# Optimization experiments

Measured on AMD Instinct MI355X. Metric: run time of the kernel, lower is better.

Reference implementation:

```python
import jax, jax.numpy as jnp
import numpy as np

B, S, D, H, DH = 2, 2048, 1024, 16, 64

def setup_inputs() -> dict:
    key = jax.random.key(0)
    ks = jax.random.split(key, 9)
    sc = 0.02
    return {
        "x":  jax.random.normal(ks[0], (B, S, D), jnp.float32),
        "Wq": jax.random.normal(ks[1], (H, D, DH), jnp.float32) * sc,
        "bq": jax.random.normal(ks[2], (H, DH), jnp.float32) * sc,
        "Wk": jax.random.normal(ks[3], (H, D, DH), jnp.float32) * sc,
        "bk": jax.random.normal(ks[4], (H, DH), jnp.float32) * sc,
        "Wv": jax.random.normal(ks[5], (H, D, DH), jnp.float32) * sc,
        "bv": jax.random.normal(ks[6], (H, DH), jnp.float32) * sc,
        "Wo": jax.random.normal(ks[7], (D, D), jnp.float32) * sc,
        "bo": jax.random.normal(ks[8], (D,), jnp.float32) * sc,
    }

def reference(x, Wq, bq, Wk, bk, Wv, bv, Wo, bo):
    # Fused version of the per-head Python loop: all H heads batched.
    # q,k,v: [B,H,S,DH]
    q = jnp.einsum("bsi,hid->bhsd", x, Wq) + bq[None, :, None, :]
    k = jnp.einsum("bsi,hid->bhsd", x, Wk) + bk[None, :, None, :]
    v = jnp.einsum("bsi,hid->bhsd", x, Wv) + bv[None, :, None, :]
    scale = 1.0 / jnp.sqrt(jnp.asarray(DH, x.dtype))
    scores = jnp.einsum("bhsd,bhtd->bhst", q, k) * scale  # [B,H,S,S]
    attn = jax.nn.softmax(scores, axis=-1)
    o = jnp.einsum("bhst,bhtd->bhsd", attn, v)            # [B,H,S,DH]
    # torch.cat([head_0,...,head_{H-1}], dim=-1) -> [B,S,H*DH]
    o = jnp.transpose(o, (0, 2, 1, 3)).reshape(B, S, H * DH)
    # Dropout is identity in eval mode; final dense projection.
    return jnp.einsum("bsi,io->bso", o, Wo) + bo
```

## Files before the change

### kernel.cpp

```cpp
#include <hip/hip_runtime.h>
#include <hip/hip_bf16.h>

#define BB 2
#define SS 2048
#define DD 1024
#define HH 16
#define DHH 64

typedef __attribute__((ext_vector_type(8))) __bf16 bf16x8;
typedef __attribute__((ext_vector_type(4))) float f32x4;
typedef __attribute__((ext_vector_type(16))) float f32x16;
typedef __attribute__((ext_vector_type(4))) int i32x4;
typedef __attribute__((ext_vector_type(4))) unsigned int u32x4;

#define MFMA16 __builtin_amdgcn_mfma_f32_16x16x32_bf16
#define MFMA32 __builtin_amdgcn_mfma_f32_32x32x16_bf16

__device__ __forceinline__ unsigned short f2b(float f) {
  __hip_bfloat16 h = __float2bfloat16(f);
  unsigned short u;
  __builtin_memcpy(&u, &h, 2);
  return u;
}

__device__ __forceinline__ float b2f(unsigned short u) {
  unsigned int x = ((unsigned int)u) << 16;
  float f;
  __builtin_memcpy(&f, &x, 4);
  return f;
}

__device__ __forceinline__ float exp2_fast(float x) {
  float r;
  asm("v_exp_f32 %0, %1" : "=v"(r) : "v"(x));
  return r;
}

__device__ __forceinline__ unsigned int cvtpk_bf16(float lo_, float hi_) {
  unsigned int r;
  asm("v_cvt_pk_bf16_f32 %0, %1, %2" : "=v"(r) : "v"(lo_), "v"(hi_));
  return r;
}

__device__ __forceinline__ void gl_lds16(const void* g, void* l) {
  __builtin_amdgcn_global_load_lds((const __attribute__((address_space(1))) void*)g,
                                   (__attribute__((address_space(3))) void*)l, 16, 0, 0);
}

__global__ __launch_bounds__(256) void k_prep(const float* __restrict__ x,
                                              const float* __restrict__ Wq,
                                              const float* __restrict__ Wk,
                                              const float* __restrict__ Wv,
                                              const float* __restrict__ Wo,
                                              unsigned short* __restrict__ xb,
                                              unsigned short* __restrict__ wqkvt,
                                              unsigned short* __restrict__ wot) {
  int blk = blockIdx.x;
  if (blk < 4096) {
    int i = blk * 256 + threadIdx.x;
    float4 v = ((const float4*)x)[i];
    ushort4 o;
    o.x = f2b(v.x); o.y = f2b(v.y); o.z = f2b(v.z); o.w = f2b(v.w);
    ((ushort4*)xb)[i] = o;
    return;
  }
  __shared__ float t[32][33];
  const float* im;
  unsigned short* om;
  int R, C, c0, r0;
  if (blk < 7168) {
    int bi2 = blk - 4096;
    int z = bi2 >> 6, rem = bi2 & 63;
    im = (z < 16 ? Wq : (z < 32 ? Wk : Wv)) + (size_t)(z & 15) * DD * DHH;
    om = wqkvt + (size_t)z * DD * DHH;
    R = DD; C = DHH;
    c0 = (rem & 1) * 32; r0 = (rem >> 1) * 32;
  } else {
    int bi2 = blk - 7168;
    im = Wo; om = wot;
    R = DD; C = DD;
    c0 = (bi2 & 31) * 32; r0 = (bi2 >> 5) * 32;
  }
  int tx = threadIdx.x & 31, ty = threadIdx.x >> 5;
#pragma unroll
  for (int rr = ty; rr < 32; rr += 8)
    t[rr][tx] = im[(size_t)(r0 + rr) * C + c0 + tx];
  __syncthreads();
#pragma unroll
  for (int rr = ty; rr < 32; rr += 8)
    om[(size_t)(c0 + rr) * R + r0 + tx] = f2b(t[tx][rr]);
}

__global__ __launch_bounds__(256) void k_qkv(const unsigned short* __restrict__ A,
                                             const unsigned short* __restrict__ Wt,
                                             const float* __restrict__ bq,
                                             const float* __restrict__ bk,
                                             const float* __restrict__ bv,
                                             unsigned short* __restrict__ Qb,
                                             unsigned short* __restrict__ Kb,
                                             unsigned short* __restrict__ Vtb) {
  __shared__ __align__(16) unsigned short SMEM[128 * 64 + 64 * 64];
  unsigned short* As = SMEM;
  unsigned short* Bs = SMEM + 128 * 64;
  int tid = threadIdx.x;
  int w = tid >> 6, l = tid & 63, lr = l & 15, lg = l >> 4;
  int col0 = blockIdx.x * 64, row0 = blockIdx.y * 128;
  int sel = col0 >> 10;
  bool vsel = (sel == 2);
  const float* biasp = sel == 0 ? bq : (sel == 1 ? bk : bv);
  unsigned short* outp = sel == 0 ? Qb : Kb;
  float qscale = sel == 0 ? 0.18033688011112042f : 1.0f;

  int r8 = l >> 3, c8 = l & 7;
  const unsigned short* Ab = A + (size_t)(row0 + w * 32 + r8) * DD + c8 * 8;
  const unsigned short* Bb = Wt + (size_t)(col0 + w * 16 + r8) * DD + c8 * 8;

  f32x4 zero = {0.f, 0.f, 0.f, 0.f};
  f32x4 acc[2][4];
#pragma unroll
  for (int m = 0; m < 2; m++)
#pragma unroll
    for (int n = 0; n < 4; n++) acc[m][n] = zero;

  for (int k0 = 0; k0 < DD; k0 += 64) {
    __syncthreads();
#pragma unroll
    for (int c = 0; c < 4; c++)
      gl_lds16(Ab + (size_t)c * 8 * DD + k0, (char*)As + (w * 32 + c * 8) * 128);
#pragma unroll
    for (int c = 0; c < 2; c++)
      gl_lds16(Bb + (size_t)c * 8 * DD + k0, (char*)Bs + (w * 16 + c * 8) * 128);
    __syncthreads();
#pragma unroll
    for (int kk = 0; kk < 2; kk++) {
      bf16x8 af[2], bfr[4];
#pragma unroll
      for (int m = 0; m < 2; m++)
        af[m] = *(const bf16x8*)&As[(w * 32 + m * 16 + lr) * 64 + kk * 32 + lg * 8];
#pragma unroll
      for (int n = 0; n < 4; n++)
        bfr[n] = *(const bf16x8*)&Bs[(n * 16 + lr) * 64 + kk * 32 + lg * 8];
      if (!vsel) {
#pragma unroll
        for (int m = 0; m < 2; m++)
#pragma unroll
          for (int n = 0; n < 4; n++)
            acc[m][n] = MFMA16(af[m], bfr[n], acc[m][n], 0, 0, 0);
      } else {
#pragma unroll
        for (int m = 0; m < 2; m++)
#pragma unroll
          for (int n = 0; n < 4; n++)
            acc[m][n] = MFMA16(bfr[n], af[m], acc[m][n], 0, 0, 0);
      }
    }
  }

  __syncthreads();
  unsigned short* Ts = SMEM;
  if (!vsel) {
#pragma unroll
    for (int n = 0; n < 4; n++) {
      int cl = n * 16 + lr;
      float bias = biasp[(col0 + cl) & 1023];
#pragma unroll
      for (int m = 0; m < 2; m++) {
#pragma unroll
        for (int j = 0; j < 4; j++) {
          int sl = w * 32 + m * 16 + lg * 4 + j;
          Ts[sl * 72 + cl] = f2b((acc[m][n][j] + bias) * qscale);
        }
      }
    }
    __syncthreads();
    int trow = tid >> 3, tc = tid & 7;
#pragma unroll
    for (int pass = 0; pass < 4; pass++) {
      int sl = pass * 32 + trow;
      int c0l = tc * 8;
      i32x4 v = *(const i32x4*)&Ts[sl * 72 + c0l];
      int c = col0 + c0l;
      int hh = (c >> 6) & 15, d = c & 63;
      int row = row0 + sl;
      int b = row >> 11, s = row & 2047;
      *(i32x4*)(outp + ((size_t)(b * HH + hh) * SS + s) * DHH + d) = v;
    }
  } else {
#pragma unroll
    for (int n = 0; n < 4; n++) {
#pragma unroll
      for (int j = 0; j < 4; j++) {
        int cl = n * 16 + lg * 4 + j;
        float bias = bv[((col0 & 1023) + cl) & 1023];
#pragma unroll
        for (int m = 0; m < 2; m++) {
          int sl = w * 32 + m * 16 + lr;
          Ts[cl * 136 + sl] = f2b(acc[m][n][j] + bias);
        }
      }
    }
    __syncthreads();
    int trow = tid >> 4, tc = tid & 15;
    int b = row0 >> 11, s0 = row0 & 2047;
#pragma unroll
    for (int pass = 0; pass < 4; pass++) {
      int cl = pass * 16 + trow;
      int s8 = tc * 8;
      i32x4 v = *(const i32x4*)&Ts[cl * 136 + s8];
      int cg = (col0 & 1023) + cl;
      *(i32x4*)(Vtb + (size_t)(b * 1024 + cg) * SS + s0 + s8) = v;
    }
  }
}

__global__ __launch_bounds__(256) void k_proj(const unsigned short* __restrict__ A,
                                              const unsigned short* __restrict__ Wt,
                                              const float* __restrict__ bo,
                                              float* __restrict__ out) {
  __shared__ __align__(16) unsigned short As[64 * 64];
  __shared__ __align__(16) unsigned short Bs[64 * 64];
  int tid = threadIdx.x;
  int w = tid >> 6, l = tid & 63, lr = l & 15, lg = l >> 4;
  int col0 = blockIdx.x * 64, row0 = blockIdx.y * 64;

  int r8 = l >> 3, c8 = l & 7;
  const unsigned short* Ab = A + (size_t)(row0 + w * 16 + r8) * DD + c8 * 8;
  const unsigned short* Bb = Wt + (size_t)(col0 + w * 16 + r8) * DD + c8 * 8;

  f32x4 zero = {0.f, 0.f, 0.f, 0.f};
  f32x4 acc[4];
#pragma unroll
  for (int n = 0; n < 4; n++) acc[n] = zero;

  for (int k0 = 0; k0 < DD; k0 += 64) {
    __syncthreads();
#pragma unroll
    for (int c = 0; c < 2; c++) {
      gl_lds16(Ab + (size_t)c * 8 * DD + k0, (char*)As + (w * 16 + c * 8) * 128);
      gl_lds16(Bb + (size_t)c * 8 * DD + k0, (char*)Bs + (w * 16 + c * 8) * 128);
    }
    __syncthreads();
#pragma unroll
    for (int kk = 0; kk < 2; kk++) {
      bf16x8 af = *(const bf16x8*)&As[(w * 16 + lr) * 64 + kk * 32 + lg * 8];
      bf16x8 bfr[4];
#pragma unroll
      for (int n = 0; n < 4; n++)
        bfr[n] = *(const bf16x8*)&Bs[(n * 16 + lr) * 64 + kk * 32 + lg * 8];
#pragma unroll
      for (int n = 0; n < 4; n++)
        acc[n] = MFMA16(af, bfr[n], acc[n], 0, 0, 0);
    }
  }

#pragma unroll
  for (int n = 0; n < 4; n++) {
    int c = col0 + n * 16 + lr;
    float bias = bo[c];
#pragma unroll
    for (int j = 0; j < 4; j++) {
      int row = row0 + w * 16 + lg * 4 + j;
      out[(size_t)row * DD + c] = acc[n][j] + bias;
    }
  }
}

#define QT 128
#define KVB 64

__global__ __launch_bounds__(256, 4) void k_attn(const unsigned short* __restrict__ Q,
                                                 const unsigned short* __restrict__ K,
                                                 const unsigned short* __restrict__ Vt,
                                                 unsigned short* __restrict__ Opart,
                                                 float* __restrict__ lse) {
  __shared__ __align__(16) char sm[32768];

  int tid = threadIdx.x;
  int w = tid >> 6, lane = tid & 63;
  int q32 = lane & 31, hi = lane >> 5;
  int r8 = lane >> 3, c8 = lane & 7;
  int cg = c8 ^ r8;

  int n = blockIdx.x;
  int bh = ((n & 7) << 2) | ((n >> 3) & 3);
  int rest = n >> 5;
  int q0 = (rest & 15) * QT;
  int chunk = rest >> 4;
  int kvbase = chunk * (SS / 2);

  const unsigned short* Qm = Q + (size_t)bh * SS * DHH;
  const unsigned short* Km = K + (size_t)bh * SS * DHH;
  const unsigned short* Vm = Vt + (size_t)bh * DHH * SS;

  bf16x8 qf[4];
  {
    const unsigned short* qrow = Qm + (size_t)(q0 + w * 32 + q32) * DHH + hi * 8;
#pragma unroll
    for (int ks = 0; ks < 4; ks++)
      qf[ks] = *(const bf16x8*)(qrow + ks * 16);
  }

#pragma unroll
  for (int c = 0; c < 2; c++) {
    int rr = w * 16 + c * 8 + r8;
    gl_lds16(Km + (size_t)(kvbase + rr) * DHH + cg * 8, sm + (w * 16 + c * 8) * 128);
    gl_lds16(Vm + (size_t)rr * SS + kvbase + cg * 8, sm + 16384 + (w * 16 + c * 8) * 128);
  }
  __syncthreads();

  f32x16 oacc0 = {}, oacc1 = {};
  float m_ = -1e30f, l_ = 0.f;
  const int swq = (q32 & 7) << 4;

  for (int t = 0; t < SS / 2 / KVB; t++) {
    const char* Kc = sm + (t & 1) * 8192;
    const char* Vc = sm + 16384 + (t & 1) * 8192;

    if (t + 1 < SS / 2 / KVB) {
      int kv0 = kvbase + (t + 1) * KVB;
      char* kd = sm + ((t + 1) & 1) * 8192;
      char* vd = sm + 16384 + ((t + 1) & 1) * 8192;
#pragma unroll
      for (int c = 0; c < 2; c++) {
        int rr = w * 16 + c * 8 + r8;
        gl_lds16(Km + (size_t)(kv0 + rr) * DHH + cg * 8, kd + (w * 16 + c * 8) * 128);
        gl_lds16(Vm + (size_t)rr * SS + kv0 + cg * 8, vd + (w * 16 + c * 8) * 128);
      }
    }

    f32x16 p0 = {}, p1 = {};
    __builtin_amdgcn_s_setprio(1);
#pragma unroll
    for (int ks = 0; ks < 4; ks++) {
      int co = (ks * 32 + hi * 16) ^ swq;
      bf16x8 kf0 = *(const bf16x8*)(Kc + q32 * 128 + co);
      bf16x8 kf1 = *(const bf16x8*)(Kc + (32 + q32) * 128 + co);
      p0 = MFMA32(kf0, qf[ks], p0, 0, 0, 0);
      p1 = MFMA32(kf1, qf[ks], p1, 0, 0, 0);
    }
    __builtin_amdgcn_s_setprio(0);

    float t8[8];
#pragma unroll
    for (int r = 0; r < 8; r++)
      t8[r] = fmaxf(fmaxf(p0[r], p0[r + 8]), fmaxf(p1[r], p1[r + 8]));
#pragma unroll
    for (int r = 0; r < 4; r++) t8[r] = fmaxf(t8[r], t8[r + 4]);
    float tmax = fmaxf(fmaxf(t8[0], t8[1]), fmaxf(t8[2], t8[3]));
    tmax = fmaxf(tmax, __shfl_xor(tmax, 32));

    if (__any(tmax > m_ + 8.0f)) {
      float nm = fmaxf(m_, tmax);
      float al = exp2_fast(m_ - nm);
      m_ = nm; l_ *= al;
#pragma unroll
      for (int r = 0; r < 16; r++) { oacc0[r] *= al; oacc1[r] *= al; }
    }

#pragma unroll
    for (int r = 0; r < 16; r++) p0[r] = exp2_fast(p0[r] - m_);
#pragma unroll
    for (int r = 0; r < 16; r++) p1[r] = exp2_fast(p1[r] - m_);
    float s8[8];
#pragma unroll
    for (int r = 0; r < 8; r++) s8[r] = (p0[r] + p0[r + 8]) + (p1[r] + p1[r + 8]);
#pragma unroll
    for (int r = 0; r < 4; r++) s8[r] += s8[r + 4];
    l_ += ((s8[0] + s8[1]) + (s8[2] + s8[3]));

    __builtin_amdgcn_s_setprio(1);
    u32x4 pa;
#define MKPA(PB, u) do { \
    unsigned int a0 = cvtpk_bf16(PB[8*(u)+0], PB[8*(u)+1]); \
    unsigned int a1 = cvtpk_bf16(PB[8*(u)+2], PB[8*(u)+3]); \
    unsigned int b0 = cvtpk_bf16(PB[8*(u)+4], PB[8*(u)+5]); \
    unsigned int b1 = cvtpk_bf16(PB[8*(u)+6], PB[8*(u)+7]); \
    asm("v_permlane32_swap_b32 %0, %1" : "+v"(a0), "+v"(b0)); \
    asm("v_permlane32_swap_b32 %0, %1" : "+v"(a1), "+v"(b1)); \
    pa[0] = a0; pa[1] = a1; pa[2] = b0; pa[3] = b1; \
  } while (0)
#define PVSTEP(s) do { \
    bf16x8 pf = *(bf16x8*)&pa; \
    bf16x8 vf0 = *(const bf16x8*)(Vc + q32 * 128 + (((s) * 32 + hi * 16) ^ swq)); \
    bf16x8 vf1 = *(const bf16x8*)(Vc + (32 + q32) * 128 + (((s) * 32 + hi * 16) ^ swq)); \
    oacc0 = MFMA32(vf0, pf, oacc0, 0, 0, 0); \
    oacc1 = MFMA32(vf1, pf, oacc1, 0, 0, 0); \
  } while (0)
    MKPA(p0, 0); PVSTEP(0);
    MKPA(p0, 1); PVSTEP(1);
    MKPA(p1, 0); PVSTEP(2);
    MKPA(p1, 1); PVSTEP(3);
#undef MKPA
#undef PVSTEP
    __builtin_amdgcn_s_setprio(0);

    __syncthreads();
  }

  l_ += __shfl_xor(l_, 32);
  float invl = 1.0f / l_;
  float lsev = m_ + __log2f(l_);
  __syncthreads();
  unsigned short* Os = (unsigned short*)sm;
  int rowq = w * 32 + q32;
#pragma unroll
  for (int r = 0; r < 16; r++) {
    int d = (r & 3) + 8 * (r >> 2) + 4 * hi;
    Os[rowq * 72 + d] = f2b(oacc0[r] * invl);
    Os[rowq * 72 + 32 + d] = f2b(oacc1[r] * invl);
  }
  if (hi == 0) lse[((size_t)chunk * 32 + bh) * SS + q0 + rowq] = lsev;
  __syncthreads();
#pragma unroll
  for (int i = 0; i < 4; i++) {
    int ci = tid + i * 256;
    int r = ci >> 3, c = ci & 7;
    i32x4 v = *(const i32x4*)&Os[r * 72 + c * 8];
    *(i32x4*)(Opart + (((size_t)chunk * 32 + bh) * SS + q0 + r) * DHH + c * 8) = v;
  }
}

__global__ __launch_bounds__(256) void k_comb(const unsigned short* __restrict__ Opart,
                                              const float* __restrict__ lse,
                                              unsigned short* __restrict__ Ocat) {
  int g = blockIdx.x * 256 + threadIdx.x;
  int row = g >> 3;
  int d8 = (g & 7) * 8;
  int bh = row >> 11, q = row & 2047;
  int bi = bh >> 4, h = bh & 15;
  float e0 = lse[row], e1 = lse[BB * HH * SS + row];
  float mx = fmaxf(e0, e1);
  float w0 = exp2_fast(e0 - mx), w1 = exp2_fast(e1 - mx);
  float inv = 1.0f / (w0 + w1);
  w0 *= inv; w1 *= inv;
  const unsigned short* P0 = Opart + (size_t)row * DHH + d8;
  const unsigned short* P1 = P0 + (size_t)BB * HH * SS * DHH;
  ushort4 a0 = *(const ushort4*)P0, a1 = *(const ushort4*)(P0 + 4);
  ushort4 b0 = *(const ushort4*)P1, b1 = *(const ushort4*)(P1 + 4);
  ushort4 o0, o1;
  o0.x = f2b(w0 * b2f(a0.x) + w1 * b2f(b0.x));
  o0.y = f2b(w0 * b2f(a0.y) + w1 * b2f(b0.y));
  o0.z = f2b(w0 * b2f(a0.z) + w1 * b2f(b0.z));
  o0.w = f2b(w0 * b2f(a0.w) + w1 * b2f(b0.w));
  o1.x = f2b(w0 * b2f(a1.x) + w1 * b2f(b1.x));
  o1.y = f2b(w0 * b2f(a1.y) + w1 * b2f(b1.y));
  o1.z = f2b(w0 * b2f(a1.z) + w1 * b2f(b1.z));
  o1.w = f2b(w0 * b2f(a1.w) + w1 * b2f(b1.w));
  unsigned short* op = Ocat + ((size_t)(bi * SS + q)) * DD + h * DHH + d8;
  *(ushort4*)op = o0;
  *(ushort4*)(op + 4) = o1;
}

extern "C" void kernel_launch(void* const* d_in, const int* in_sizes, int n_in,
                              void* d_out, int out_size, void* d_ws, size_t ws_size,
                              hipStream_t stream) {
  const float* x  = (const float*)d_in[0];
  const float* Wq = (const float*)d_in[1];
  const float* bq = (const float*)d_in[2];
  const float* Wk = (const float*)d_in[3];
  const float* bk = (const float*)d_in[4];
  const float* Wv = (const float*)d_in[5];
  const float* bv = (const float*)d_in[6];
  const float* Wo = (const float*)d_in[7];
  const float* bo = (const float*)d_in[8];
  float* out = (float*)d_out;

  char* ws = (char*)d_ws;
  unsigned short* xb    = (unsigned short*)(ws);
  unsigned short* wqkvt = (unsigned short*)(ws + (size_t)(8u  << 20));
  unsigned short* wot   = (unsigned short*)(ws + (size_t)(14u << 20));
  unsigned short* Qb    = (unsigned short*)(ws + (size_t)(16u << 20));
  unsigned short* Kb    = (unsigned short*)(ws + (size_t)(24u << 20));
  unsigned short* Vt    = (unsigned short*)(ws + (size_t)(32u << 20));
  unsigned short* Ocat  = (unsigned short*)(ws + (size_t)(40u << 20));
  unsigned short* Opart = (unsigned short*)(ws + (size_t)(48u << 20));
  float*          lse   = (float*)(ws + (size_t)(64u << 20));

  k_prep<<<8192, 256, 0, stream>>>(x, Wq, Wk, Wv, Wo, xb, wqkvt, wot);
  k_qkv<<<dim3(3 * DD / 64, BB * SS / 128), 256, 0, stream>>>(xb, wqkvt, bq, bk, bv, Qb, Kb, Vt);
  k_attn<<<dim3(1024), 256, 0, stream>>>(Qb, Kb, Vt, Opart, lse);
  k_comb<<<dim3(2048), 256, 0, stream>>>(Opart, lse, Ocat);
  k_proj<<<dim3(DD / 64, BB * SS / 64), 256, 0, stream>>>(Ocat, wot, bo, out);
}
```

Before: 133.3 us.

## Double-buffer LDS tiles in QKV and output projection GEMMs

Both projection GEMM kernels now use two shared-memory buffers and issue the global-to-LDS loads for the next K-tile before computing on the current one. The two barriers per iteration become one, so global load latency can overlap the MFMA work. In exchange, LDS use per block doubles, which may reduce occupancy. The QKV buffer stride is also padded to 12288 elements.

```diff
diff --git a/kernel.cpp b/kernel.cpp
--- a/kernel.cpp
+++ b/kernel.cpp
@@ -99,9 +99,7 @@
                                              unsigned short* __restrict__ Qb,
                                              unsigned short* __restrict__ Kb,
                                              unsigned short* __restrict__ Vtb) {
-  __shared__ __align__(16) unsigned short SMEM[128 * 64 + 64 * 64];
-  unsigned short* As = SMEM;
-  unsigned short* Bs = SMEM + 128 * 64;
+  __shared__ __align__(16) unsigned short SMEM[2 * 12288];
   int tid = threadIdx.x;
   int w = tid >> 6, l = tid & 63, lr = l & 15, lg = l >> 4;
   int col0 = blockIdx.x * 64, row0 = blockIdx.y * 128;
@@ -122,15 +120,24 @@
 #pragma unroll
     for (int n = 0; n < 4; n++) acc[m][n] = zero;
 
-  for (int k0 = 0; k0 < DD; k0 += 64) {
-    __syncthreads();
-#pragma unroll
-    for (int c = 0; c < 4; c++)
-      gl_lds16(Ab + (size_t)c * 8 * DD + k0, (char*)As + (w * 32 + c * 8) * 128);
-#pragma unroll
-    for (int c = 0; c < 2; c++)
-      gl_lds16(Bb + (size_t)c * 8 * DD + k0, (char*)Bs + (w * 16 + c * 8) * 128);
-    __syncthreads();
+#define QKV_STAGE(T) do { \
+    unsigned short* buf_ = SMEM + ((T) & 1) * 12288; \
+    int k0_ = (T) * 64; \
+    _Pragma("unroll") \
+    for (int c = 0; c < 4; c++) \
+      gl_lds16(Ab + (size_t)c * 8 * DD + k0_, (char*)buf_ + (w * 32 + c * 8) * 128); \
+    _Pragma("unroll") \
+    for (int c = 0; c < 2; c++) \
+      gl_lds16(Bb + (size_t)c * 8 * DD + k0_, (char*)(buf_ + 8192) + (w * 16 + c * 8) * 128); \
+  } while (0)
+
+  QKV_STAGE(0);
+  __syncthreads();
+
+  for (int t = 0; t < 16; t++) {
+    const unsigned short* As = SMEM + (t & 1) * 12288;
+    const unsigned short* Bs = As + 8192;
+    if (t + 1 < 16) QKV_STAGE(t + 1);
 #pragma unroll
     for (int kk = 0; kk < 2; kk++) {
       bf16x8 af[2], bfr[4];
@@ -154,9 +161,10 @@
             acc[m][n] = MFMA16(bfr[n], af[m], acc[m][n], 0, 0, 0);
       }
     }
-  }
-
-  __syncthreads();
+    __syncthreads();
+  }
+#undef QKV_STAGE
+
   unsigned short* Ts = SMEM;
   if (!vsel) {
 #pragma unroll
@@ -217,8 +225,7 @@
                                               const unsigned short* __restrict__ Wt,
                                               const float* __restrict__ bo,
                                               float* __restrict__ out) {
-  __shared__ __align__(16) unsigned short As[64 * 64];
-  __shared__ __align__(16) unsigned short Bs[64 * 64];
+  __shared__ __align__(16) unsigned short SMEM[2 * 8192];
   int tid = threadIdx.x;
   int w = tid >> 6, l = tid & 63, lr = l & 15, lg = l >> 4;
   int col0 = blockIdx.x * 64, row0 = blockIdx.y * 64;
@@ -232,14 +239,23 @@
 #pragma unroll
   for (int n = 0; n < 4; n++) acc[n] = zero;
 
-  for (int k0 = 0; k0 < DD; k0 += 64) {
-    __syncthreads();
-#pragma unroll
-    for (int c = 0; c < 2; c++) {
-      gl_lds16(Ab + (size_t)c * 8 * DD + k0, (char*)As + (w * 16 + c * 8) * 128);
-      gl_lds16(Bb + (size_t)c * 8 * DD + k0, (char*)Bs + (w * 16 + c * 8) * 128);
-    }
-    __syncthreads();
+#define PROJ_STAGE(T) do { \
+    unsigned short* buf_ = SMEM + ((T) & 1) * 8192; \
+    int k0_ = (T) * 64; \
+    _Pragma("unroll") \
+    for (int c = 0; c < 2; c++) { \
+      gl_lds16(Ab + (size_t)c * 8 * DD + k0_, (char*)buf_ + (w * 16 + c * 8) * 128); \
+      gl_lds16(Bb + (size_t)c * 8 * DD + k0_, (char*)(buf_ + 4096) + (w * 16 + c * 8) * 128); \
+    } \
+  } while (0)
+
+  PROJ_STAGE(0);
+  __syncthreads();
+
+  for (int t = 0; t < 16; t++) {
+    const unsigned short* As = SMEM + (t & 1) * 8192;
+    const unsigned short* Bs = As + 4096;
+    if (t + 1 < 16) PROJ_STAGE(t + 1);
 #pragma unroll
     for (int kk = 0; kk < 2; kk++) {
       bf16x8 af = *(const bf16x8*)&As[(w * 16 + lr) * 64 + kk * 32 + lg * 8];
@@ -251,7 +267,9 @@
       for (int n = 0; n < 4; n++)
         acc[n] = MFMA16(af, bfr[n], acc[n], 0, 0, 0);
     }
-  }
+    __syncthreads();
+  }
+#undef PROJ_STAGE
 
 #pragma unroll
   for (int n = 0; n < 4; n++) {
```

Result: faster. 126.2 us, median of 2 (-5.3%).
